# Kernel optimization log

Measured on AMD Instinct MI355X. Metric: run time of the kernel, lower is better.

## Reference

```python
import jax, jax.numpy as jnp
import numpy as np

NUM_ENTITY = 100000
NUM_TYPE = 5000
DIM = 128
BATCH = 512
MARGIN = 2.0


def setup_inputs() -> dict:
    key = jax.random.key(0)
    k1, k2, k3 = jax.random.split(key, 3)
    x_batch = jax.random.randint(k1, (BATCH,), 0, NUM_ENTITY)
    # xavier_uniform-style init for embedding tables
    lim_e = float(np.sqrt(6.0 / (NUM_ENTITY + DIM)))
    lim_t = float(np.sqrt(6.0 / (NUM_TYPE + DIM)))
    ent_table = jax.random.uniform(k2, (NUM_ENTITY, DIM), minval=-lim_e, maxval=lim_e, dtype=jnp.float32)
    type_table = jax.random.uniform(k3, (NUM_TYPE, DIM), minval=-lim_t, maxval=lim_t, dtype=jnp.float32)
    # padding_idx=0 rows are zero in torch Embedding
    ent_table = ent_table.at[0].set(0.0)
    type_table = type_table.at[0].set(0.0)
    return {"ent_table": ent_table, "type_table": type_table, "x_batch": x_batch}


def reference(ent_table, type_table, x_batch):
    # [B, D] entity embedding lookup
    e = ent_table[x_batch]
    # L1 distance from each entity to every type embedding: [B, T]
    dist = jnp.sum(jnp.abs(e[:, None, :] - type_table[None, :, :]), axis=2)
    return jax.nn.sigmoid(MARGIN - dist)
```

## Files before the change

kernel.cpp:

```cpp
#include <hip/hip_runtime.h>
#include <math.h>

#define NUM_ENTITY 100000
#define NUM_TYPE   5000
#define DIM        128
#define BATCH      512
#define MARGIN     2.0f

#define BT 32
#define TT 32
#define ESTRIDE 132
#define PSTRIDE 68

__global__ __launch_bounds__(256) void l1dist_sigmoid_kernel(
    const float* __restrict__ ent,
    const float* __restrict__ typ,
    const int*   __restrict__ xb,
    float*       __restrict__ out)
{
    __shared__ float smem[2 * BT * ESTRIDE];
    float* eT = smem;
    float* tT = smem + BT * ESTRIDE;

    const int tid = threadIdx.x;
    const int l   = tid & 63;
    const int w   = tid >> 6;
    const int tx  = l & 7;
    const int ty  = l >> 3;
    const int b0  = blockIdx.y * BT;
    const int t0  = blockIdx.x * TT;

#pragma unroll
    for (int s = 0; s < 4; ++s) {
        const int g = tid + 256 * s;
        const int row = g >> 5, c4 = g & 31;
        const int er = xb[b0 + row];
        *(float4*)&eT[row * ESTRIDE + c4 * 4] =
            *(const float4*)&ent[er * DIM + c4 * 4];
    }
#pragma unroll
    for (int s = 0; s < 4; ++s) {
        const int g = tid + 256 * s;
        const int row = g >> 5, c4 = g & 31;
        const int tr = min(t0 + row, NUM_TYPE - 1);
        *(float4*)&tT[row * ESTRIDE + c4 * 4] =
            *(const float4*)&typ[tr * DIM + c4 * 4];
    }
    __syncthreads();

    float acc[4][4] = {};
    const int kbase = w * 32;
#pragma unroll
    for (int ks = 0; ks < 8; ++ks) {
        float4 ev[4], tv[4];
#pragma unroll
        for (int i = 0; i < 4; ++i)
            ev[i] = *(const float4*)&eT[(ty + 8 * i) * ESTRIDE + kbase + 4 * ks];
#pragma unroll
        for (int j = 0; j < 4; ++j)
            tv[j] = *(const float4*)&tT[(tx + 8 * j) * ESTRIDE + kbase + 4 * ks];
#pragma unroll
        for (int i = 0; i < 4; ++i)
#pragma unroll
            for (int j = 0; j < 4; ++j) {
                acc[i][j] += fabsf(ev[i].x - tv[j].x);
                acc[i][j] += fabsf(ev[i].y - tv[j].y);
                acc[i][j] += fabsf(ev[i].z - tv[j].z);
                acc[i][j] += fabsf(ev[i].w - tv[j].w);
            }
    }
    __syncthreads();

    float* part = smem;
#pragma unroll
    for (int i = 0; i < 4; ++i) {
        float4 v;
        v.x = acc[i][0]; v.y = acc[i][1]; v.z = acc[i][2]; v.w = acc[i][3];
        *(float4*)&part[l * PSTRIDE + w * 16 + i * 4] = v;
    }
    __syncthreads();

    float4 sum;
    sum.x = 0.0f; sum.y = 0.0f; sum.z = 0.0f; sum.w = 0.0f;
#pragma unroll
    for (int wp = 0; wp < 4; ++wp) {
        const float4 v = *(const float4*)&part[l * PSTRIDE + wp * 16 + w * 4];
        sum.x += v.x; sum.y += v.y; sum.z += v.z; sum.w += v.w;
    }

    const int b = b0 + ty + 8 * w;
    const float d[4] = {sum.x, sum.y, sum.z, sum.w};
#pragma unroll
    for (int j = 0; j < 4; ++j) {
        const int t = t0 + tx + 8 * j;
        if (t < NUM_TYPE) {
            const float x = MARGIN - d[j];
            out[b * NUM_TYPE + t] = 1.0f / (1.0f + __expf(-x));
        }
    }
}

extern "C" void kernel_launch(void* const* d_in, const int* in_sizes, int n_in,
                              void* d_out, int out_size, void* d_ws, size_t ws_size,
                              hipStream_t stream) {
    const float* ent = (const float*)d_in[0];
    const float* typ = (const float*)d_in[1];
    const int*   xb  = (const int*)d_in[2];
    float*       out = (float*)d_out;

    dim3 grid((NUM_TYPE + TT - 1) / TT, BATCH / BT);
    dim3 block(256);
    l1dist_sigmoid_kernel<<<grid, block, 0, stream>>>(ent, typ, xb, out);
}
```

Before: 31.41 us.

## Compute L1 distance in packed fp16 with fdot2 accumulation

Entity and type tiles are converted to fp16 when staged into shared memory. The inner loop then does packed half2 subtraction, clears the sign bit with a mask, and accumulates into fp32 with the fdot2 builtin against ones. This halves shared-memory traffic and cuts the per-element ALU op count. In exchange the differences are rounded to fp16 before being summed, which may reduce accuracy.

Result: faster. 25.75 us (-18.0%).

```diff
diff --git a/kernel.cpp b/kernel.cpp
--- a/kernel.cpp
+++ b/kernel.cpp
@@ -9,8 +9,12 @@
 
 #define BT 32
 #define TT 32
-#define ESTRIDE 132
+#define HSTRIDE 136
 #define PSTRIDE 68
+
+typedef _Float16 half_t;
+typedef half_t half2_t __attribute__((ext_vector_type(2)));
+typedef half_t half4_t __attribute__((ext_vector_type(4)));
 
 __global__ __launch_bounds__(256) void l1dist_sigmoid_kernel(
     const float* __restrict__ ent,
@@ -18,9 +22,9 @@
     const int*   __restrict__ xb,
     float*       __restrict__ out)
 {
-    __shared__ float smem[2 * BT * ESTRIDE];
-    float* eT = smem;
-    float* tT = smem + BT * ESTRIDE;
+    __shared__ float smem[2 * BT * HSTRIDE / 2];
+    half_t* eH = (half_t*)smem;
+    half_t* tH = (half_t*)smem + BT * HSTRIDE;
 
     const int tid = threadIdx.x;
     const int l   = tid & 63;
@@ -35,38 +39,63 @@
         const int g = tid + 256 * s;
         const int row = g >> 5, c4 = g & 31;
         const int er = xb[b0 + row];
-        *(float4*)&eT[row * ESTRIDE + c4 * 4] =
-            *(const float4*)&ent[er * DIM + c4 * 4];
+        const float4 v = *(const float4*)&ent[er * DIM + c4 * 4];
+        half4_t hv = {(half_t)v.x, (half_t)v.y, (half_t)v.z, (half_t)v.w};
+        *(half4_t*)&eH[row * HSTRIDE + c4 * 4] = hv;
     }
 #pragma unroll
     for (int s = 0; s < 4; ++s) {
         const int g = tid + 256 * s;
         const int row = g >> 5, c4 = g & 31;
         const int tr = min(t0 + row, NUM_TYPE - 1);
-        *(float4*)&tT[row * ESTRIDE + c4 * 4] =
-            *(const float4*)&typ[tr * DIM + c4 * 4];
+        const float4 v = *(const float4*)&typ[tr * DIM + c4 * 4];
+        half4_t hv = {(half_t)v.x, (half_t)v.y, (half_t)v.z, (half_t)v.w};
+        *(half4_t*)&tH[row * HSTRIDE + c4 * 4] = hv;
     }
     __syncthreads();
 
+    const half2_t ones = {(half_t)1.0f, (half_t)1.0f};
     float acc[4][4] = {};
     const int kbase = w * 32;
+
+#if __has_builtin(__builtin_amdgcn_fdot2)
+#define ABS_DOT2(EU, TU, ACC)                                                  \
+    {                                                                          \
+        half2_t _d = __builtin_bit_cast(half2_t, (EU)) -                       \
+                     __builtin_bit_cast(half2_t, (TU));                        \
+        unsigned _du = __builtin_bit_cast(unsigned, _d) & 0x7fff7fffu;         \
+        ACC = __builtin_amdgcn_fdot2(__builtin_bit_cast(half2_t, _du), ones,   \
+                                     ACC, false);                              \
+    }
+#else
+#define ABS_DOT2(EU, TU, ACC)                                                  \
+    {                                                                          \
+        half2_t _d = __builtin_bit_cast(half2_t, (EU)) -                       \
+                     __builtin_bit_cast(half2_t, (TU));                        \
+        unsigned _du = __builtin_bit_cast(unsigned, _d) & 0x7fff7fffu;         \
+        half2_t _a = __builtin_bit_cast(half2_t, _du);                         \
+        ACC += (float)_a[0] + (float)_a[1];                                    \
+    }
+#endif
+
 #pragma unroll
-    for (int ks = 0; ks < 8; ++ks) {
-        float4 ev[4], tv[4];
+    for (int ks = 0; ks < 4; ++ks) {
+        const int kk = kbase + 8 * ks;
+        uint4 ev[4], tv[4];
 #pragma unroll
         for (int i = 0; i < 4; ++i)
-            ev[i] = *(const float4*)&eT[(ty + 8 * i) * ESTRIDE + kbase + 4 * ks];
+            ev[i] = *(const uint4*)&eH[(ty + 8 * i) * HSTRIDE + kk];
 #pragma unroll
         for (int j = 0; j < 4; ++j)
-            tv[j] = *(const float4*)&tT[(tx + 8 * j) * ESTRIDE + kbase + 4 * ks];
+            tv[j] = *(const uint4*)&tH[(tx + 8 * j) * HSTRIDE + kk];
 #pragma unroll
         for (int i = 0; i < 4; ++i)
 #pragma unroll
             for (int j = 0; j < 4; ++j) {
-                acc[i][j] += fabsf(ev[i].x - tv[j].x);
-                acc[i][j] += fabsf(ev[i].y - tv[j].y);
-                acc[i][j] += fabsf(ev[i].z - tv[j].z);
-                acc[i][j] += fabsf(ev[i].w - tv[j].w);
+                ABS_DOT2(ev[i].x, tv[j].x, acc[i][j])
+                ABS_DOT2(ev[i].y, tv[j].y, acc[i][j])
+                ABS_DOT2(ev[i].z, tv[j].z, acc[i][j])
+                ABS_DOT2(ev[i].w, tv[j].w, acc[i][j])
             }
     }
     __syncthreads();
```
